# Performance work log

Measured on AMD Instinct MI355X. Metric: run time of the kernel, lower is better.

The kernel has to match this reference:

```python
import jax, jax.numpy as jnp
import numpy as np

N = 50000       # nodes
E_RND = 750000  # random edges (plus N self-loops)
IN = 512        # in_dim
HID = 64        # hidden_dim
H = 4           # num_heads
L = 2           # blk_size
OUT = 64        # out_dim
NEG = 0.01      # leaky_relu slope (torch default)
ATT_NEG = 0.2   # attention leaky_relu slope (GAT convention)


def setup_inputs() -> dict:
    key = jax.random.key(0)
    ks = jax.random.split(key, 12)
    sl = jnp.arange(N, dtype=jnp.int32)
    src = jnp.concatenate([jax.random.randint(ks[0], (E_RND,), 0, N, dtype=jnp.int32), sl])
    dst = jnp.concatenate([jax.random.randint(ks[1], (E_RND,), 0, N, dtype=jnp.int32), sl])
    ft = jax.random.normal(ks[2], (N, IN), jnp.float32)
    s = lambda f: np.float32(1.0 / np.sqrt(f))
    Wp = jax.random.normal(ks[3], (IN, HID), jnp.float32) * s(IN)
    We = jax.random.normal(ks[4], (HID, HID), jnp.float32) * s(HID)
    a_l = jax.random.normal(ks[5], (L, H, HID), jnp.float32) * s(HID)
    a_r = jax.random.normal(ks[6], (L, H, HID), jnp.float32) * s(HID)
    Wv = jax.random.normal(ks[7], (L, H, HID, HID), jnp.float32) * s(HID)
    Wg_pool = jax.random.normal(ks[8], (L, HID, HID), jnp.float32) * s(HID)
    Wgate = jax.random.normal(ks[9], (L, 3 * HID, H), jnp.float32) * s(3 * HID)
    bgate = jnp.zeros((L, H), jnp.float32)
    Wtran = jax.random.normal(ks[10], (HID * (H + 1), OUT), jnp.float32) * s(HID * (H + 1))
    btran = jnp.zeros((OUT,), jnp.float32)
    return dict(ft=ft, Wp=Wp, We=We, a_l=a_l, a_r=a_r, Wv=Wv, Wg_pool=Wg_pool,
                Wgate=Wgate, bgate=bgate, Wtran=Wtran, btran=btran, src=src, dst=dst)


def _segment_softmax(e, seg, n):
    m = jax.ops.segment_max(e, seg, num_segments=n)
    ex = jnp.exp(e - m[seg])
    s = jax.ops.segment_sum(ex, seg, num_segments=n)
    return ex / s[seg]


def reference(ft, Wp, We, a_l, a_r, Wv, Wg_pool, Wgate, bgate, Wtran, btran, src, dst):
    proj_feat = ft @ Wp                       # [N,HID]
    deg = jax.ops.segment_sum(jnp.ones_like(dst, jnp.float32), dst, num_segments=N)  # [N]
    cur = proj_feat
    for i in range(L):
        proj_z = cur @ We                     # [N,HID] shared attention embedding
        # per-head additive attention logits
        el = jnp.einsum('nd,hd->nh', proj_z, a_l[i])
        er = jnp.einsum('nd,hd->nh', proj_z, a_r[i])
        e = jax.nn.leaky_relu(el[src] + er[dst], ATT_NEG)        # [E,H]
        alpha = _segment_softmax(e, dst, N)                      # [E,H]
        vals = jnp.einsum('nd,hdo->nho', cur, Wv[i])             # [N,H,HID]
        msg = alpha[:, :, None] * vals[src]                      # [E,H,HID]
        agg = jax.ops.segment_sum(msg, dst, num_segments=N)      # [N,H,HID]
        # GaAN gate: [v_i, max-pool of projected neighbor v, mean of neighbor v]
        pooled = cur @ Wg_pool[i]                                # [N,HID]
        mx = jax.ops.segment_max(pooled[src], dst, num_segments=N)
        mn = jax.ops.segment_sum(cur[src], dst, num_segments=N) / deg[:, None]
        gate_in = jnp.concatenate([cur, mx, mn], axis=-1)        # [N,3*HID]
        g = jax.nn.sigmoid(gate_in @ Wgate[i] + bgate[i])        # [N,H]
        agg = agg * g[:, :, None]
        merged = agg.mean(axis=1) if i < L - 1 else agg.reshape(N, H * HID)
        cur = jax.nn.leaky_relu(merged, NEG)
    h = jnp.concatenate([proj_feat, cur], axis=-1)               # [N,HID*(H+1)]
    return h @ Wtran + btran                                     # [N,OUT]
```

## Files before the change

kernel.cpp:

```cpp
#include <hip/hip_runtime.h>
#include <hip/hip_fp16.h>

#define NN 50000
#define EE 800000
#define IND 512
#define HD 64
#define NB_SCAN 49

__device__ __forceinline__ float lrelu(float x, float s){ return x > 0.f ? x : s*x; }

__global__ void k_deg(const int* __restrict__ dst, int* __restrict__ deg){
  int e = blockIdx.x*256 + threadIdx.x;
  if(e < EE) atomicAdd(&deg[dst[e]], 1);
}

__global__ void k_scan1(const int* __restrict__ deg, int* __restrict__ psum){
  __shared__ int sh[256];
  int base = blockIdx.x*1024 + threadIdx.x*4;
  int s = 0;
  #pragma unroll
  for(int j=0;j<4;j++){ int i=base+j; if(i<NN) s += deg[i]; }
  sh[threadIdx.x]=s; __syncthreads();
  for(int st=128; st>0; st>>=1){ if(threadIdx.x<st) sh[threadIdx.x]+=sh[threadIdx.x+st]; __syncthreads(); }
  if(threadIdx.x==0) psum[blockIdx.x]=sh[0];
}

__global__ void k_scan2(int* __restrict__ psum, int nb){
  if(threadIdx.x==0){ int acc=0; for(int i=0;i<nb;i++){ int v=psum[i]; psum[i]=acc; acc+=v; } psum[nb]=acc; }
}

__global__ void k_scan3(const int* __restrict__ deg, const int* __restrict__ psum, int* __restrict__ rowp){
  __shared__ int sh[256];
  int t = threadIdx.x;
  int base = blockIdx.x*1024 + t*4;
  int v[4]; int s=0;
  #pragma unroll
  for(int j=0;j<4;j++){ int i=base+j; v[j] = (i<NN)?deg[i]:0; s+=v[j]; }
  sh[t]=s; __syncthreads();
  for(int st=1; st<256; st<<=1){
    int add = (t>=st)? sh[t-st] : 0;
    __syncthreads();
    sh[t] += add;
    __syncthreads();
  }
  int excl = sh[t]-s + psum[blockIdx.x];
  #pragma unroll
  for(int j=0;j<4;j++){ int i=base+j; if(i<NN){ rowp[i]=excl; excl+=v[j]; } }
  if(blockIdx.x==0 && t==0) rowp[NN] = psum[NB_SCAN];
}

__global__ void k_fill(const int* __restrict__ src, const int* __restrict__ dst,
                       const int* __restrict__ rowp, int* __restrict__ cnt, int* __restrict__ csrc){
  int e = blockIdx.x*256 + threadIdx.x;
  if(e < EE){
    int d = dst[e];
    int p = atomicAdd(&cnt[d], 1);
    csrc[rowp[d] + p] = src[e];
  }
}

__global__ void k_prew(const float* __restrict__ We, const float* __restrict__ al,
                       const float* __restrict__ ar, float* __restrict__ w_elr){
  int t = blockIdx.x*256 + threadIdx.x;
  if(t >= 1024) return;
  int layer = t>>9, o = (t>>6)&7, k = t&63;
  const float* a = (o<4 ? al : ar) + layer*256 + (o&3)*64;
  const float* w = We + k*64;
  float s = 0.f;
  for(int d2=0; d2<64; ++d2) s += w[d2]*a[d2];
  w_elr[t] = s;
}

__device__ __forceinline__ void load_A_tile(const float* __restrict__ A, int row0, int lda, int kcol0, float* As){
  int t = threadIdx.x;
  int lr = t>>2;
  int lc = (t&3)*16;
  float4 a0,a1,a2,a3;
  int row = row0 + lr;
  if(row < NN){
    const float* ap = A + (size_t)row*lda + kcol0 + lc;
    a0=*(const float4*)ap; a1=*(const float4*)(ap+4); a2=*(const float4*)(ap+8); a3=*(const float4*)(ap+12);
  } else {
    a0=a1=a2=a3=make_float4(0.f,0.f,0.f,0.f);
  }
  float* d = As + (size_t)lc*68 + lr;
  d[0*68]=a0.x;  d[1*68]=a0.y;  d[2*68]=a0.z;  d[3*68]=a0.w;
  d[4*68]=a1.x;  d[5*68]=a1.y;  d[6*68]=a1.z;  d[7*68]=a1.w;
  d[8*68]=a2.x;  d[9*68]=a2.y;  d[10*68]=a2.z; d[11*68]=a2.w;
  d[12*68]=a3.x; d[13*68]=a3.y; d[14*68]=a3.z; d[15*68]=a3.w;
}

__device__ __forceinline__ void load_B_tile(const float* __restrict__ B, int krow0, float* Bs){
  int t = threadIdx.x;
  int bk = t>>2; int lc = (t&3)*16;
  const float* bp = B + (size_t)(krow0+bk)*64 + lc;
  *(float4*)(Bs + bk*64 + lc)      = *(const float4*)bp;
  *(float4*)(Bs + bk*64 + lc + 4)  = *(const float4*)(bp+4);
  *(float4*)(Bs + bk*64 + lc + 8)  = *(const float4*)(bp+8);
  *(float4*)(Bs + bk*64 + lc + 12) = *(const float4*)(bp+12);
}

__device__ __forceinline__ void tile64_compute(const float* __restrict__ As, const float* __restrict__ Bs,
                                               float acc[4][4], int ty, int tx){
  #pragma unroll 4
  for(int kk=0; kk<64; kk++){
    float4 a = *(const float4*)(As + kk*68 + ty*4);
    float4 b = *(const float4*)(Bs + kk*64 + tx*4);
    acc[0][0]+=a.x*b.x; acc[0][1]+=a.x*b.y; acc[0][2]+=a.x*b.z; acc[0][3]+=a.x*b.w;
    acc[1][0]+=a.y*b.x; acc[1][1]+=a.y*b.y; acc[1][2]+=a.y*b.z; acc[1][3]+=a.y*b.w;
    acc[2][0]+=a.z*b.x; acc[2][1]+=a.z*b.y; acc[2][2]+=a.z*b.z; acc[2][3]+=a.z*b.w;
    acc[3][0]+=a.w*b.x; acc[3][1]+=a.w*b.y; acc[3][2]+=a.w*b.z; acc[3][3]+=a.w*b.w;
  }
}

__global__ __launch_bounds__(256, 4) void k_gemm_proj(const float* __restrict__ A, const float* __restrict__ B, float* __restrict__ C){
  __shared__ float As[64*68];
  __shared__ float Bs[64*64];
  int row0 = blockIdx.x*64;
  int ty = threadIdx.x>>4, tx = threadIdx.x&15;
  float acc[4][4] = {};
  #pragma unroll 1
  for(int kt=0; kt<IND; kt+=64){
    __syncthreads();
    load_A_tile(A, row0, IND, kt, As);
    load_B_tile(B, kt, Bs);
    __syncthreads();
    tile64_compute(As, Bs, acc, ty, tx);
  }
  #pragma unroll
  for(int i=0;i<4;i++){
    int row = row0 + ty*4 + i;
    if(row < NN) *(float4*)(C + (size_t)row*64 + tx*4) = make_float4(acc[i][0],acc[i][1],acc[i][2],acc[i][3]);
  }
}

__global__ __launch_bounds__(256, 4) void k_nodemm_pack(const float* __restrict__ cur, const float* __restrict__ Wg,
                                                        __half2* __restrict__ pack){
  __shared__ float As[64*68];
  __shared__ float Bs[64*64];
  int row0 = blockIdx.x*64;
  int ty = threadIdx.x>>4, tx = threadIdx.x&15;
  load_A_tile(cur, row0, 64, 0, As);
  load_B_tile(Wg, 0, Bs);
  __syncthreads();
  float acc[4][4] = {};
  tile64_compute(As, Bs, acc, ty, tx);
  #pragma unroll
  for(int i=0;i<4;i++){
    int row = row0 + ty*4 + i;
    if(row < NN){
      union { uint4 u; __half2 h[4]; } pk;
      #pragma unroll
      for(int j=0;j<4;j++){
        float cv = As[(tx*4+j)*68 + ty*4 + i];
        pk.h[j] = __floats2half2_rn(cv, acc[i][j]);
      }
      *(uint4*)(pack + (size_t)row*64 + tx*4) = pk.u;
    }
  }
}

__global__ __launch_bounds__(256) void k_eler2(const float* __restrict__ cur, const float* __restrict__ w_elr,
                                               float* __restrict__ el, float* __restrict__ er){
  int wid = threadIdx.x>>6, lane = threadIdx.x&63;
  int n = blockIdx.x*4 + wid;
  if(n >= NN) return;
  float c = cur[(size_t)n*64 + lane];
  #pragma unroll
  for(int o=0; o<8; o++){
    float p = c * w_elr[o*64 + lane];
    #pragma unroll
    for(int st=32; st; st>>=1) p += __shfl_xor(p, st, 64);
    if(lane==0){
      if(o<4) el[(size_t)n*4 + o] = p;
      else    er[(size_t)n*4 + o-4] = p;
    }
  }
}

__global__ __launch_bounds__(256) void k_edge(const int* __restrict__ rowp, const int* __restrict__ csrc,
    const float* __restrict__ el, const float* __restrict__ er, const float* __restrict__ cur,
    const __half2* __restrict__ pack,
    const float* __restrict__ Wg, const float* __restrict__ bg, float* __restrict__ aggcg)
{
  __shared__ int    ssh[4][64];
  __shared__ float4 xsh[4][64];
  int wid = threadIdx.x>>6, lane = threadIdx.x&63;
  int d = blockIdx.x*4 + wid;
  if(d >= NN) return;
  int e0 = rowp[d], e1 = rowp[d+1];
  float4 erd = *(const float4*)(er + (size_t)d*4);
  float n0=0,n1=0,n2=0,n3=0, den0=0,den1=0,den2=0,den3=0, mn=0, mxp=-1e30f;

  for(int c=e0; c<e1; c+=64){
    int jmax = min(64, e1-c);
    float x0=0.f, x1=0.f, x2=0.f, x3=0.f; int s=0;
    if(lane < jmax){
      s = csrc[c+lane];
      float4 ev = *(const float4*)(el + (size_t)s*4);
      x0 = __expf(lrelu(ev.x+erd.x, 0.2f));
      x1 = __expf(lrelu(ev.y+erd.y, 0.2f));
      x2 = __expf(lrelu(ev.z+erd.z, 0.2f));
      x3 = __expf(lrelu(ev.w+erd.w, 0.2f));
      den0+=x0; den1+=x1; den2+=x2; den3+=x3;
    }
    ssh[wid][lane] = s;
    xsh[wid][lane] = make_float4(x0,x1,x2,x3);
    for(int j=0; j<jmax; ++j){
      int sj = __builtin_amdgcn_readfirstlane(ssh[wid][j]);
      float4 xj = xsh[wid][j];
      float2 f = __half22float2(pack[(size_t)sj*64 + lane]);
      n0 += xj.x*f.x; n1 += xj.y*f.x; n2 += xj.z*f.x; n3 += xj.w*f.x;
      mn += f.x;
      mxp = fmaxf(mxp, f.y);
    }
  }
  #pragma unroll
  for(int st=32; st; st>>=1){
    den0+=__shfl_xor(den0,st,64); den1+=__shfl_xor(den1,st,64);
    den2+=__shfl_xor(den2,st,64); den3+=__shfl_xor(den3,st,64);
  }
  float cd  = cur[(size_t)d*64 + lane];
  float mnn = mn / (float)(e1-e0);
  float4 w0 = *(const float4*)(Wg + lane*4);
  float4 w1 = *(const float4*)(Wg + (64+lane)*4);
  float4 w2 = *(const float4*)(Wg + (128+lane)*4);
  float g0 = cd*w0.x + mxp*w1.x + mnn*w2.x;
  float g1 = cd*w0.y + mxp*w1.y + mnn*w2.y;
  float g2 = cd*w0.z + mxp*w1.z + mnn*w2.z;
  float g3 = cd*w0.w + mxp*w1.w + mnn*w2.w;
  #pragma unroll
  for(int st=32; st; st>>=1){
    g0+=__shfl_xor(g0,st,64); g1+=__shfl_xor(g1,st,64);
    g2+=__shfl_xor(g2,st,64); g3+=__shfl_xor(g3,st,64);
  }
  g0 = 1.f/(1.f+__expf(-(g0+bg[0])));
  g1 = 1.f/(1.f+__expf(-(g1+bg[1])));
  g2 = 1.f/(1.f+__expf(-(g2+bg[2])));
  g3 = 1.f/(1.f+__expf(-(g3+bg[3])));
  float* od = aggcg + (size_t)d*256;
  od[lane]       = g0 * n0/den0;
  od[64 + lane]  = g1 * n1/den1;
  od[128 + lane] = g2 * n2/den2;
  od[192 + lane] = g3 * n3/den3;
}

__global__ __launch_bounds__(256, 4) void k_post0(const float* __restrict__ A, const float* __restrict__ B, float* __restrict__ C){
  __shared__ float As[64*68];
  __shared__ float Bs[64*64];
  int row0 = blockIdx.x*64;
  int ty = threadIdx.x>>4, tx = threadIdx.x&15;
  float acc[4][4] = {};
  #pragma unroll 1
  for(int kt=0; kt<256; kt+=64){
    __syncthreads();
    load_A_tile(A, row0, 256, kt, As);
    load_B_tile(B, kt, Bs);
    __syncthreads();
    tile64_compute(As, Bs, acc, ty, tx);
  }
  #pragma unroll
  for(int i=0;i<4;i++){
    int row = row0 + ty*4 + i;
    if(row < NN) *(float4*)(C + (size_t)row*64 + tx*4) =
      make_float4(lrelu(0.25f*acc[i][0],0.01f), lrelu(0.25f*acc[i][1],0.01f),
                  lrelu(0.25f*acc[i][2],0.01f), lrelu(0.25f*acc[i][3],0.01f));
  }
}

__global__ __launch_bounds__(256, 4) void k_final2(const float* __restrict__ pf, const float* __restrict__ aggcg,
                                                   const float* __restrict__ Wv1, const float* __restrict__ Wt,
                                                   const float* __restrict__ bt, float* __restrict__ C){
  __shared__ float As[64*68];
  __shared__ float Bs[64*64];
  int row0 = blockIdx.x*64;
  int ty = threadIdx.x>>4, tx = threadIdx.x&15;
  float accF[4][4] = {};
  load_A_tile(pf, row0, 64, 0, As);
  load_B_tile(Wt, 0, Bs);
  __syncthreads();
  tile64_compute(As, Bs, accF, ty, tx);
  #pragma unroll 1
  for(int h=0; h<4; ++h){
    __syncthreads();
    load_A_tile(aggcg + h*64, row0, 256, 0, As);
    load_B_tile(Wv1 + (size_t)h*4096, 0, Bs);
    __syncthreads();
    float acc1[4][4] = {};
    tile64_compute(As, Bs, acc1, ty, tx);
    __syncthreads();
    #pragma unroll
    for(int i=0;i<4;i++)
      #pragma unroll
      for(int j=0;j<4;j++)
        As[(tx*4+j)*68 + ty*4 + i] = lrelu(acc1[i][j], 0.01f);
    load_B_tile(Wt, 64 + h*64, Bs);
    __syncthreads();
    tile64_compute(As, Bs, accF, ty, tx);
  }
  float4 bias = *(const float4*)(bt + tx*4);
  #pragma unroll
  for(int i=0;i<4;i++){
    int row = row0 + ty*4 + i;
    if(row < NN){
      *(float4*)(C + (size_t)row*64 + tx*4) =
        make_float4(accF[i][0]+bias.x, accF[i][1]+bias.y, accF[i][2]+bias.z, accF[i][3]+bias.w);
    }
  }
}

extern "C" void kernel_launch(void* const* d_in, const int* in_sizes, int n_in,
                              void* d_out, int out_size, void* d_ws, size_t ws_size,
                              hipStream_t stream) {
  const float* ft    = (const float*)d_in[0];
  const float* Wp    = (const float*)d_in[1];
  const float* We    = (const float*)d_in[2];
  const float* a_l   = (const float*)d_in[3];
  const float* a_r   = (const float*)d_in[4];
  const float* Wv    = (const float*)d_in[5];
  const float* Wgp   = (const float*)d_in[6];
  const float* Wgate = (const float*)d_in[7];
  const float* bgate = (const float*)d_in[8];
  const float* Wtran = (const float*)d_in[9];
  const float* btran = (const float*)d_in[10];
  const int*   src   = (const int*)d_in[11];
  const int*   dst   = (const int*)d_in[12];
  float* out = (float*)d_out;

  char* p = (char*)d_ws;
  auto alloc = [&](size_t bytes)->char* { char* r = p; p += (bytes + 255) & ~(size_t)255; return r; };
  int* deg  = (int*)alloc((size_t)NN*4);
  int* cnt  = (int*)alloc((size_t)NN*4);
  int* rowp = (int*)alloc((size_t)(NN+1)*4);
  int* psum = (int*)alloc(64*4);
  int* csrc = (int*)alloc((size_t)EE*4);
  float*   pf    = (float*)alloc((size_t)NN*64*4);
  float*   cur1  = (float*)alloc((size_t)NN*64*4);
  float*   elb   = (float*)alloc((size_t)NN*4*4);
  float*   erb   = (float*)alloc((size_t)NN*4*4);
  __half2* pack  = (__half2*)alloc((size_t)NN*64*4);
  float*   aggcg = (float*)alloc((size_t)NN*256*4);
  float*   welr  = (float*)alloc(1024*4);

  hipMemsetAsync(deg, 0, (size_t)NN*4, stream);
  hipMemsetAsync(cnt, 0, (size_t)NN*4, stream);
  k_deg<<<(EE+255)/256, 256, 0, stream>>>(dst, deg);
  k_scan1<<<NB_SCAN, 256, 0, stream>>>(deg, psum);
  k_scan2<<<1, 64, 0, stream>>>(psum, NB_SCAN);
  k_scan3<<<NB_SCAN, 256, 0, stream>>>(deg, psum, rowp);
  k_fill<<<(EE+255)/256, 256, 0, stream>>>(src, dst, rowp, cnt, csrc);
  k_prew<<<4, 256, 0, stream>>>(We, a_l, a_r, welr);

  k_gemm_proj<<<(NN+63)/64, 256, 0, stream>>>(ft, Wp, pf);

  int gb = (NN+63)/64;
  k_nodemm_pack<<<gb, 256, 0, stream>>>(pf, Wgp, pack);
  k_eler2<<<NN/4, 256, 0, stream>>>(pf, welr, elb, erb);
  k_edge<<<NN/4, 256, 0, stream>>>(rowp, csrc, elb, erb, pf, pack, Wgate, bgate, aggcg);
  k_post0<<<gb, 256, 0, stream>>>(aggcg, Wv, cur1);
  k_nodemm_pack<<<gb, 256, 0, stream>>>(cur1, Wgp + 4096, pack);
  k_eler2<<<NN/4, 256, 0, stream>>>(cur1, welr + 512, elb, erb);
  k_edge<<<NN/4, 256, 0, stream>>>(rowp, csrc, elb, erb, cur1, pack, Wgate + 768, bgate + 4, aggcg);
  k_final2<<<gb, 256, 0, stream>>>(pf, aggcg, Wv + 16384, Wtran, btran, out);
}
```

Baseline: 632.4 us.

## Fuse el/er projection into pack kernel, merge small kernels, relayout A tile

Fuses the per-node attention logit computation (el/er) into the node GEMM pack kernel, with shuffle reductions across the 16 column threads, so the separate k_eler2 launches and their reread of cur are removed. Merges the psum scan and w_elr precompute into one launch and collapses two memsets into one. Changes the shared A tile from a transposed layout to row-major with vectorized stores, and the inner loop now does scalar strided LDS reads of A. Together these cut launch count and the scattered LDS writes, but the scalar A reads may cost LDS bandwidth or bank conflicts in the GEMMs.

```diff
diff --git a/kernel.cpp b/kernel.cpp
--- a/kernel.cpp
+++ b/kernel.cpp
@@ -25,8 +25,20 @@
   if(threadIdx.x==0) psum[blockIdx.x]=sh[0];
 }
 
-__global__ void k_scan2(int* __restrict__ psum, int nb){
-  if(threadIdx.x==0){ int acc=0; for(int i=0;i<nb;i++){ int v=psum[i]; psum[i]=acc; acc+=v; } psum[nb]=acc; }
+__global__ void k_scan2_prew(int* __restrict__ psum, int nb,
+                             const float* __restrict__ We, const float* __restrict__ al,
+                             const float* __restrict__ ar, float* __restrict__ w_elr){
+  if(blockIdx.x == 0){
+    if(threadIdx.x==0){ int acc=0; for(int i=0;i<nb;i++){ int v=psum[i]; psum[i]=acc; acc+=v; } psum[nb]=acc; }
+    return;
+  }
+  int t = (blockIdx.x-1)*256 + threadIdx.x;
+  int layer = t>>9, o = (t>>6)&7, k = t&63;
+  const float* a = (o<4 ? al : ar) + layer*256 + (o&3)*64;
+  const float* w = We + k*64;
+  float s = 0.f;
+  for(int d2=0; d2<64; ++d2) s += w[d2]*a[d2];
+  w_elr[t] = s;
 }
 
 __global__ void k_scan3(const int* __restrict__ deg, const int* __restrict__ psum, int* __restrict__ rowp){
@@ -57,18 +69,6 @@
     int p = atomicAdd(&cnt[d], 1);
     csrc[rowp[d] + p] = src[e];
   }
-}
-
-__global__ void k_prew(const float* __restrict__ We, const float* __restrict__ al,
-                       const float* __restrict__ ar, float* __restrict__ w_elr){
-  int t = blockIdx.x*256 + threadIdx.x;
-  if(t >= 1024) return;
-  int layer = t>>9, o = (t>>6)&7, k = t&63;
-  const float* a = (o<4 ? al : ar) + layer*256 + (o&3)*64;
-  const float* w = We + k*64;
-  float s = 0.f;
-  for(int d2=0; d2<64; ++d2) s += w[d2]*a[d2];
-  w_elr[t] = s;
 }
 
 __device__ __forceinline__ void load_A_tile(const float* __restrict__ A, int row0, int lda, int kcol0, float* As){
@@ -83,33 +83,37 @@
   } else {
     a0=a1=a2=a3=make_float4(0.f,0.f,0.f,0.f);
   }
-  float* d = As + (size_t)lc*68 + lr;
-  d[0*68]=a0.x;  d[1*68]=a0.y;  d[2*68]=a0.z;  d[3*68]=a0.w;
-  d[4*68]=a1.x;  d[5*68]=a1.y;  d[6*68]=a1.z;  d[7*68]=a1.w;
-  d[8*68]=a2.x;  d[9*68]=a2.y;  d[10*68]=a2.z; d[11*68]=a2.w;
-  d[12*68]=a3.x; d[13*68]=a3.y; d[14*68]=a3.z; d[15*68]=a3.w;
+  float* d = As + lr*68 + lc;
+  *(float4*)(d)    = a0;
+  *(float4*)(d+4)  = a1;
+  *(float4*)(d+8)  = a2;
+  *(float4*)(d+12) = a3;
 }
 
 __device__ __forceinline__ void load_B_tile(const float* __restrict__ B, int krow0, float* Bs){
   int t = threadIdx.x;
-  int bk = t>>2; int lc = (t&3)*16;
-  const float* bp = B + (size_t)(krow0+bk)*64 + lc;
-  *(float4*)(Bs + bk*64 + lc)      = *(const float4*)bp;
-  *(float4*)(Bs + bk*64 + lc + 4)  = *(const float4*)(bp+4);
-  *(float4*)(Bs + bk*64 + lc + 8)  = *(const float4*)(bp+8);
-  *(float4*)(Bs + bk*64 + lc + 12) = *(const float4*)(bp+12);
+  int r  = t>>4;
+  int c4 = (t&15)*4;
+  #pragma unroll
+  for(int m=0;m<4;m++){
+    int row = m*16 + r;
+    *(float4*)(Bs + row*64 + c4) = *(const float4*)(B + (size_t)(krow0+row)*64 + c4);
+  }
 }
 
 __device__ __forceinline__ void tile64_compute(const float* __restrict__ As, const float* __restrict__ Bs,
                                                float acc[4][4], int ty, int tx){
   #pragma unroll 4
   for(int kk=0; kk<64; kk++){
-    float4 a = *(const float4*)(As + kk*68 + ty*4);
+    float a0 = As[(ty*4+0)*68 + kk];
+    float a1 = As[(ty*4+1)*68 + kk];
+    float a2 = As[(ty*4+2)*68 + kk];
+    float a3 = As[(ty*4+3)*68 + kk];
     float4 b = *(const float4*)(Bs + kk*64 + tx*4);
-    acc[0][0]+=a.x*b.x; acc[0][1]+=a.x*b.y; acc[0][2]+=a.x*b.z; acc[0][3]+=a.x*b.w;
-    acc[1][0]+=a.y*b.x; acc[1][1]+=a.y*b.y; acc[1][2]+=a.y*b.z; acc[1][3]+=a.y*b.w;
-    acc[2][0]+=a.z*b.x; acc[2][1]+=a.z*b.y; acc[2][2]+=a.z*b.z; acc[2][3]+=a.z*b.w;
-    acc[3][0]+=a.w*b.x; acc[3][1]+=a.w*b.y; acc[3][2]+=a.w*b.z; acc[3][3]+=a.w*b.w;
+    acc[0][0]+=a0*b.x; acc[0][1]+=a0*b.y; acc[0][2]+=a0*b.z; acc[0][3]+=a0*b.w;
+    acc[1][0]+=a1*b.x; acc[1][1]+=a1*b.y; acc[1][2]+=a1*b.z; acc[1][3]+=a1*b.w;
+    acc[2][0]+=a2*b.x; acc[2][1]+=a2*b.y; acc[2][2]+=a2*b.z; acc[2][3]+=a2*b.w;
+    acc[3][0]+=a3*b.x; acc[3][1]+=a3*b.y; acc[3][2]+=a3*b.z; acc[3][3]+=a3*b.w;
   }
 }
 
@@ -134,46 +138,58 @@
   }
 }
 
-__global__ __launch_bounds__(256, 4) void k_nodemm_pack(const float* __restrict__ cur, const float* __restrict__ Wg,
-                                                        __half2* __restrict__ pack){
+__global__ __launch_bounds__(256, 4) void k_packeler(const float* __restrict__ cur, const float* __restrict__ Wg,
+                                                     const float* __restrict__ welr, __half2* __restrict__ pack,
+                                                     float* __restrict__ el, float* __restrict__ er){
   __shared__ float As[64*68];
   __shared__ float Bs[64*64];
+  __shared__ float Ws[512];
+  int t = threadIdx.x;
   int row0 = blockIdx.x*64;
-  int ty = threadIdx.x>>4, tx = threadIdx.x&15;
+  int ty = t>>4, tx = t&15;
   load_A_tile(cur, row0, 64, 0, As);
   load_B_tile(Wg, 0, Bs);
+  if(t < 128) *(float4*)(Ws + t*4) = *(const float4*)(welr + t*4);
   __syncthreads();
   float acc[4][4] = {};
   tile64_compute(As, Bs, acc, ty, tx);
+  float po[8][4];
+  #pragma unroll
+  for(int o=0;o<8;o++)
+    #pragma unroll
+    for(int i=0;i<4;i++) po[o][i] = 0.f;
   #pragma unroll
   for(int i=0;i<4;i++){
     int row = row0 + ty*4 + i;
-    if(row < NN){
-      union { uint4 u; __half2 h[4]; } pk;
+    float4 cv = make_float4(0.f,0.f,0.f,0.f);
+    if(row < NN) cv = *(const float4*)(cur + (size_t)row*64 + tx*4);
+    union { uint4 u; __half2 h[4]; } pk;
+    pk.h[0] = __floats2half2_rn(cv.x, acc[i][0]);
+    pk.h[1] = __floats2half2_rn(cv.y, acc[i][1]);
+    pk.h[2] = __floats2half2_rn(cv.z, acc[i][2]);
+    pk.h[3] = __floats2half2_rn(cv.w, acc[i][3]);
+    if(row < NN) *(uint4*)(pack + (size_t)row*64 + tx*4) = pk.u;
+    #pragma unroll
+    for(int o=0;o<8;o++){
+      float4 w = *(const float4*)(Ws + o*64 + tx*4);
+      po[o][i] += cv.x*w.x + cv.y*w.y + cv.z*w.z + cv.w*w.w;
+    }
+  }
+  #pragma unroll
+  for(int st=1; st<16; st<<=1)
+    #pragma unroll
+    for(int o=0;o<8;o++)
       #pragma unroll
-      for(int j=0;j<4;j++){
-        float cv = As[(tx*4+j)*68 + ty*4 + i];
-        pk.h[j] = __floats2half2_rn(cv, acc[i][j]);
+      for(int i=0;i<4;i++)
+        po[o][i] += __shfl_xor(po[o][i], st, 64);
+  if(tx < 8){
+    #pragma unroll
+    for(int i=0;i<4;i++){
+      int row = row0 + ty*4 + i;
+      if(row < NN){
+        if(tx < 4) el[(size_t)row*4 + tx]     = po[tx][i];
+        else       er[(size_t)row*4 + tx - 4] = po[tx][i];
       }
-      *(uint4*)(pack + (size_t)row*64 + tx*4) = pk.u;
-    }
-  }
-}
-
-__global__ __launch_bounds__(256) void k_eler2(const float* __restrict__ cur, const float* __restrict__ w_elr,
-                                               float* __restrict__ el, float* __restrict__ er){
-  int wid = threadIdx.x>>6, lane = threadIdx.x&63;
-  int n = blockIdx.x*4 + wid;
-  if(n >= NN) return;
-  float c = cur[(size_t)n*64 + lane];
-  #pragma unroll
-  for(int o=0; o<8; o++){
-    float p = c * w_elr[o*64 + lane];
-    #pragma unroll
-    for(int st=32; st; st>>=1) p += __shfl_xor(p, st, 64);
-    if(lane==0){
-      if(o<4) el[(size_t)n*4 + o] = p;
-      else    er[(size_t)n*4 + o-4] = p;
     }
   }
 }
@@ -290,10 +306,11 @@
     tile64_compute(As, Bs, acc1, ty, tx);
     __syncthreads();
     #pragma unroll
-    for(int i=0;i<4;i++)
-      #pragma unroll
-      for(int j=0;j<4;j++)
-        As[(tx*4+j)*68 + ty*4 + i] = lrelu(acc1[i][j], 0.01f);
+    for(int i=0;i<4;i++){
+      float4 v = make_float4(lrelu(acc1[i][0],0.01f), lrelu(acc1[i][1],0.01f),
+                             lrelu(acc1[i][2],0.01f), lrelu(acc1[i][3],0.01f));
+      *(float4*)(As + (ty*4+i)*68 + tx*4) = v;
+    }
     load_B_tile(Wt, 64 + h*64, Bs);
     __syncthreads();
     tile64_compute(As, Bs, accF, ty, tx);
@@ -342,24 +359,20 @@
   float*   aggcg = (float*)alloc((size_t)NN*256*4);
   float*   welr  = (float*)alloc(1024*4);
 
-  hipMemsetAsync(deg, 0, (size_t)NN*4, stream);
-  hipMemsetAsync(cnt, 0, (size_t)NN*4, stream);
+  hipMemsetAsync(deg, 0, (size_t)((char*)cnt - (char*)deg) + (size_t)NN*4, stream);
   k_deg<<<(EE+255)/256, 256, 0, stream>>>(dst, deg);
   k_scan1<<<NB_SCAN, 256, 0, stream>>>(deg, psum);
-  k_scan2<<<1, 64, 0, stream>>>(psum, NB_SCAN);
+  k_scan2_prew<<<5, 256, 0, stream>>>(psum, NB_SCAN, We, a_l, a_r, welr);
   k_scan3<<<NB_SCAN, 256, 0, stream>>>(deg, psum, rowp);
   k_fill<<<(EE+255)/256, 256, 0, stream>>>(src, dst, rowp, cnt, csrc);
-  k_prew<<<4, 256, 0, stream>>>(We, a_l, a_r, welr);
 
   k_gemm_proj<<<(NN+63)/64, 256, 0, stream>>>(ft, Wp, pf);
 
   int gb = (NN+63)/64;
-  k_nodemm_pack<<<gb, 256, 0, stream>>>(pf, Wgp, pack);
-  k_eler2<<<NN/4, 256, 0, stream>>>(pf, welr, elb, erb);
+  k_packeler<<<gb, 256, 0, stream>>>(pf, Wgp, welr, pack, elb, erb);
   k_edge<<<NN/4, 256, 0, stream>>>(rowp, csrc, elb, erb, pf, pack, Wgate, bgate, aggcg);
   k_post0<<<gb, 256, 0, stream>>>(aggcg, Wv, cur1);
-  k_nodemm_pack<<<gb, 256, 0, stream>>>(cur1, Wgp + 4096, pack);
-  k_eler2<<<NN/4, 256, 0, stream>>>(cur1, welr + 512, elb, erb);
+  k_packeler<<<gb, 256, 0, stream>>>(cur1, Wgp + 4096, welr + 512, pack, elb, erb);
   k_edge<<<NN/4, 256, 0, stream>>>(rowp, csrc, elb, erb, cur1, pack, Wgate + 768, bgate + 4, aggcg);
   k_final2<<<gb, 256, 0, stream>>>(pf, aggcg, Wv + 16384, Wtran, btran, out);
 }
```

Result: faster. 564.5 us (-10.7%).
